# Performance work log

Hardware: AMD Instinct MI355X
Metric: run time of the kernel (lower is better)

Reference implementation:

```python
import jax, jax.numpy as jnp
import numpy as np
import math

N, V, NH = 4096, 256, 64  # samples, variables (channels), hidden units


def _permutation_skeleton(v):
    # perm[c] is a (V, V-1) selection matrix keeping all variables j != c,
    # columns ordered by j (faithful to CustomizedRelaModule.permutation_matrix
    # with skeleton = 1 - I, so max_dim = V - 1 and no zero-padding remains).
    perm = np.zeros((v, v, v - 1), dtype=np.float32)
    for c in range(v):
        idx = np.delete(np.arange(v), c)
        perm[c, idx, np.arange(v - 1)] = 1.0
    return jnp.asarray(perm)


def setup_inputs() -> dict:
    key = jax.random.key(0)
    k = jax.random.split(key, 7)
    data = jax.random.normal(k[0], (N, V), dtype=jnp.float32)
    adj = jax.random.normal(k[1], (V, V), dtype=jnp.float32)        # self.adj_matrix ~ N(0,1)
    neurons = jax.random.normal(k[2], (NH, V), dtype=jnp.float32)   # self.neurons ~ N(0,1)
    s1 = 1.0 / math.sqrt(V - 1)  # input_layer: uniform(-1/sqrt(in), 1/sqrt(in)), in = max_dim = V-1
    w_in = jax.random.uniform(k[3], (V, V - 1, NH), minval=-s1, maxval=s1, dtype=jnp.float32)
    b_in = jax.random.uniform(k[4], (V, NH), minval=-s1, maxval=s1, dtype=jnp.float32)
    s2 = 1.0 / math.sqrt(NH)
    w_out = jax.random.uniform(k[5], (V, NH, 1), minval=-s2, maxval=s2, dtype=jnp.float32)
    b_out = jax.random.uniform(k[6], (V, 1), minval=-s2, maxval=s2, dtype=jnp.float32)
    perm = _permutation_skeleton(V)
    return {"data": data, "adj": adj, "neurons": neurons,
            "w_in": w_in, "b_in": b_in, "w_out": w_out, "b_out": b_out,
            "perm": perm}


def reference(data, adj, neurons, w_in, b_in, w_out, b_out, perm):
    # categorical_matrix is identity, so the adjacency passed is adj itself.
    # Linear3D input layer with adj + permutation:
    #   masked[n, c, k] = sum_j data[n, j] * adj[j, c] * perm[c, j, k]
    # i.e. per channel c, gather adj-weighted inputs for all j != c.
    masked = jnp.einsum('nj,jc,cjk->nck', data, adj, perm)  # (N, V, V-1)
    # per-channel linear + tanh
    h = jnp.tanh(jnp.einsum('nck,ckh->nch', masked, w_in) + b_in[None])  # (N, V, NH)
    # output Linear3D with adj_matrix = neurons (NH, V): elementwise gate then per-channel linear
    gated = h * neurons.T[None]  # (N, V, NH)
    out = jnp.einsum('nch,cho->nco', gated, w_out) + b_out[None]  # (N, V, 1)
    return (adj, out[..., 0])
```

## Files before the change

kernel.cpp:

```cpp
#include <hip/hip_runtime.h>
#include <hip/hip_bf16.h>

#define NS   4096
#define NV   256
#define NHID 64
#define K2F  2.8853900817779268f

typedef short s8v __attribute__((ext_vector_type(8)));
typedef float f4v __attribute__((ext_vector_type(4)));

typedef __attribute__((address_space(1))) const unsigned int GU;
typedef __attribute__((address_space(3))) unsigned int LU;

__device__ __forceinline__ void gload16(const void* gp, void* lp) {
    __builtin_amdgcn_global_load_lds((GU*)gp, (LU*)lp, 16, 0, 0);
}

__device__ __forceinline__ unsigned short f2bf(float x) {
    __hip_bfloat16 h = __float2bfloat16(x);
    return *reinterpret_cast<unsigned short*>(&h);
}

__global__ __launch_bounds__(256) void k_prep_all(
        const float* __restrict__ adj, const float* __restrict__ w_in,
        unsigned short* __restrict__ W2t,
        const float* __restrict__ data, unsigned short* __restrict__ dataB,
        float* __restrict__ out0,
        const float* __restrict__ neurons, const float* __restrict__ w_out,
        const float* __restrict__ b_out, float* __restrict__ g2, float* __restrict__ BO,
        const float* __restrict__ b_in, float* __restrict__ bi2)
{
    __shared__ float t[64][65];
    const int blk = blockIdx.x, tid = threadIdx.x;
    if (blk < 1024) {
        int c  = blk >> 2;
        int k0 = (blk & 3) * 64;
#pragma unroll
        for (int i = 0; i < 16; ++i) {
            int lin = i * 256 + tid;
            int kr = lin >> 6, h = lin & 63;
            int k = k0 + kr;
            float v = 0.0f;
            if (k != c) {
                int m = k - (k > c ? 1 : 0);
                v = adj[k * NV + c] * w_in[((size_t)c * 255 + m) * 64 + h];
            }
            t[kr][h] = v;
        }
        __syncthreads();
#pragma unroll
        for (int i = 0; i < 16; ++i) {
            int lin = i * 256 + tid;
            int h = lin >> 6, kr = lin & 63;
            W2t[((size_t)(c * 64 + h)) * NV + k0 + kr] = f2bf(t[kr][h]);
        }
        return;
    }
    const int b = blk - 1024;
    if (b < 1024) {
        int i = b * 256 + tid;
        float4 v = reinterpret_cast<const float4*>(data)[i];
        ushort4 o = make_ushort4(f2bf(v.x), f2bf(v.y), f2bf(v.z), f2bf(v.w));
        reinterpret_cast<ushort4*>(dataB)[i] = o;
    } else if (b < 1088) {
        int i = (b - 1024) * 256 + tid;
        reinterpret_cast<float4*>(out0)[i] = reinterpret_cast<const float4*>(adj)[i];
    } else if (b < 1152) {
        int j = (b - 1088) * 256 + tid;
        int c = j >> 6, h = j & 63;
        float gv = neurons[h * NV + c] * w_out[j];
        g2[j] = 2.0f * gv;
        float s = gv;
        s += __shfl_xor(s, 1);  s += __shfl_xor(s, 2);  s += __shfl_xor(s, 4);
        s += __shfl_xor(s, 8);  s += __shfl_xor(s, 16); s += __shfl_xor(s, 32);
        if ((tid & 63) == 0) BO[c] = b_out[c] + s;
    } else {
        int i = (b - 1152) * 256 + tid;
        float4 v = reinterpret_cast<const float4*>(b_in)[i];
        v.x *= K2F; v.y *= K2F; v.z *= K2F; v.w *= K2F;
        reinterpret_cast<float4*>(bi2)[i] = v;
    }
}

__global__ __launch_bounds__(256, 3) void k_gemm_fused(
        const unsigned short* __restrict__ dataB,
        const unsigned short* __restrict__ W2t,
        const float* __restrict__ g2,
        const float* __restrict__ bi2,
        const float* __restrict__ BO,
        float* __restrict__ out1)
{
    __shared__ __align__(16) char lds[49152];
    const int tid  = threadIdx.x;
    const int w    = tid >> 6;
    const int lane = tid & 63;
    const int lq   = lane >> 4, lr = lane & 15;
    const int wr   = w >> 1, wc = w & 1;

    const int orig = (int)blockIdx.x;
    const int swz  = (orig & 7) * 512 + (orig >> 3);
    const int bm0  = (swz & 31) << 7;
    const int bn0  = (swz >> 5) << 7;

    f4v acc[4][4];
#pragma unroll
    for (int mi = 0; mi < 4; ++mi)
#pragma unroll
        for (int ni = 0; ni < 4; ++ni)
            acc[mi][ni] = (f4v){0.f, 0.f, 0.f, 0.f};

    const char* dA = (const char*)dataB;
    const char* dB = (const char*)W2t;
    const int rowt = tid >> 2;
    const int colb = (tid & 3) * 16;
    const char* srcA = dA + (size_t)(bm0 + rowt) * 512 + colb;
    const char* srcB = dB + (size_t)(bn0 + rowt) * 512 + colb;
    const unsigned ldst = (unsigned)(rowt * 64 + colb);

#define STAGE(KT, BUFO)                                                        \
    do {                                                                       \
        gload16(srcA + (KT) * 64,         lds + (BUFO) + ldst);                \
        gload16(srcA + 32768 + (KT) * 64, lds + (BUFO) + 4096 + ldst);         \
        gload16(srcB + (KT) * 64,         lds + (BUFO) + 8192 + ldst);         \
        gload16(srcB + 32768 + (KT) * 64, lds + (BUFO) + 12288 + ldst);        \
    } while (0)

    STAGE(0, 0);
    STAGE(1, 16384);

#pragma unroll
    for (int kt = 0; kt < 8; ++kt) {
        const int bufo = (kt % 3) * 16384;
        if (kt < 7) { asm volatile("s_waitcnt vmcnt(4)" ::: "memory"); }
        else        { asm volatile("s_waitcnt vmcnt(0)" ::: "memory"); }
        __builtin_amdgcn_sched_barrier(0);
        __builtin_amdgcn_s_barrier();
        __builtin_amdgcn_sched_barrier(0);
        if (kt < 6) STAGE(kt + 2, ((kt + 2) % 3) * 16384);

        s8v afr[4], bfr[4];
#pragma unroll
        for (int mi = 0; mi < 4; ++mi) {
            int ml = wr * 64 + mi * 16 + lr;
            afr[mi] = *reinterpret_cast<const s8v*>(lds + bufo + ml * 64 + lq * 16);
        }
#pragma unroll
        for (int ni = 0; ni < 4; ++ni) {
            int nl = wc * 64 + ni * 16 + lr;
            bfr[ni] = *reinterpret_cast<const s8v*>(lds + bufo + 8192 + nl * 64 + lq * 16);
        }
        __builtin_amdgcn_s_setprio(1);
#pragma unroll
        for (int mi = 0; mi < 4; ++mi)
#pragma unroll
            for (int ni = 0; ni < 4; ++ni)
                acc[mi][ni] = __builtin_amdgcn_mfma_f32_16x16x32_bf16(
                    bfr[ni], afr[mi], acc[mi][ni], 0, 0, 0);
        __builtin_amdgcn_s_setprio(0);
    }
#undef STAGE

    const int cidx = (bn0 >> 6) + wc;
    float4 g2v[4], bi2v[4];
#pragma unroll
    for (int ni = 0; ni < 4; ++ni) {
        int base = cidx * 64 + ni * 16 + lq * 4;
        g2v[ni]  = *(const float4*)&g2 [base];
        bi2v[ni] = *(const float4*)&bi2[base];
    }
    const float BOv = BO[cidx];

    float s0, s1, s2, s3;
#define EPI_TERM(T, GC, BC, RR)                                                \
    { float mm = __builtin_fmaf(acc[mi][ni][RR], K2F, (BC));                   \
      float e  = __builtin_amdgcn_exp2f(mm);                                   \
      (T) = __builtin_fmaf((GC), __builtin_amdgcn_rcpf(e + 1.0f), (T)); }
#define EPI_MI(T)                                                              \
    { float t = 0.f;                                                           \
      _Pragma("unroll")                                                        \
      for (int ni = 0; ni < 4; ++ni) {                                         \
          EPI_TERM(t, g2v[ni].x, bi2v[ni].x, 0);                               \
          EPI_TERM(t, g2v[ni].y, bi2v[ni].y, 1);                               \
          EPI_TERM(t, g2v[ni].z, bi2v[ni].z, 2);                               \
          EPI_TERM(t, g2v[ni].w, bi2v[ni].w, 3);                               \
      }                                                                        \
      t += __shfl_xor(t, 16);                                                  \
      t += __shfl_xor(t, 32);                                                  \
      (T) = t; }
    { const int mi = 0; EPI_MI(s0); }
    { const int mi = 1; EPI_MI(s1); }
    { const int mi = 2; EPI_MI(s2); }
    { const int mi = 3; EPI_MI(s3); }
#undef EPI_MI
#undef EPI_TERM
    float v = lane < 16 ? s0 : (lane < 32 ? s1 : (lane < 48 ? s2 : s3));
    out1[(unsigned)(bm0 + wr * 64 + lane) * NV + cidx] = BOv - v;
}

extern "C" void kernel_launch(void* const* d_in, const int* in_sizes, int n_in,
                              void* d_out, int out_size, void* d_ws, size_t ws_size,
                              hipStream_t stream) {
    const float* data    = (const float*)d_in[0];
    const float* adj     = (const float*)d_in[1];
    const float* neurons = (const float*)d_in[2];
    const float* w_in    = (const float*)d_in[3];
    const float* b_in    = (const float*)d_in[4];
    const float* w_out   = (const float*)d_in[5];
    const float* b_out   = (const float*)d_in[6];

    float* out0 = (float*)d_out;
    float* out1 = out0 + NV * NV;

    unsigned short* dataB = (unsigned short*)d_ws;
    unsigned short* W2t   = (unsigned short*)((char*)d_ws + 2097152);
    float*          g2    = (float*)((char*)d_ws + 10485760);
    float*          bi2   = (float*)((char*)d_ws + 10551296);
    float*          BO    = (float*)((char*)d_ws + 10616832);

    hipLaunchKernelGGL(k_prep_all, dim3(2192), dim3(256), 0, stream,
                       adj, w_in, W2t, data, dataB, out0,
                       neurons, w_out, b_out, g2, BO, b_in, bi2);
    hipLaunchKernelGGL(k_gemm_fused, dim3(4096), dim3(256), 0, stream,
                       dataB, W2t, g2, bi2, BO, out1);
}
```

Measured before the change: 60.02 us.

## Use 64-wide K tiles with XOR-swizzled LDS and double buffering

The GEMM main loop now stages 128-byte K slices (64 bf16) per tile instead of 64-byte slices, running 4 iterations instead of 8. It uses two 32 KB buffers instead of three 16 KB ones. The LDS rows are XOR-swizzled by row index to avoid bank conflicts on the 16-byte fragment reads. The change also adds a second barrier per iteration before refilling the just-consumed buffer, and raises LDS use to 64 KB per block, which may reduce occupancy below the launch-bounds target of 3 blocks.

```diff
diff --git a/kernel.cpp b/kernel.cpp
--- a/kernel.cpp
+++ b/kernel.cpp
@@ -90,7 +90,7 @@
         const float* __restrict__ BO,
         float* __restrict__ out1)
 {
-    __shared__ __align__(16) char lds[49152];
+    __shared__ __align__(16) char lds[65536];
     const int tid  = threadIdx.x;
     const int w    = tid >> 6;
     const int lane = tid & 63;
@@ -109,54 +109,71 @@
         for (int ni = 0; ni < 4; ++ni)
             acc[mi][ni] = (f4v){0.f, 0.f, 0.f, 0.f};
 
+    unsigned int offA[4], offB[4], ldso[4];
+#pragma unroll
+    for (int t = 0; t < 4; ++t) {
+        int o = w * 4096 + t * 1024 + lane * 16;
+        int row = o >> 7;
+        int inner = (o & 127) ^ ((row & 7) << 4);
+        ldso[t] = (unsigned)(w * 4096 + t * 1024);
+        offA[t] = (unsigned)(bm0 + row) * 512u + (unsigned)inner;
+        offB[t] = (unsigned)(bn0 + row) * 512u + (unsigned)inner;
+    }
+
     const char* dA = (const char*)dataB;
     const char* dB = (const char*)W2t;
-    const int rowt = tid >> 2;
-    const int colb = (tid & 3) * 16;
-    const char* srcA = dA + (size_t)(bm0 + rowt) * 512 + colb;
-    const char* srcB = dB + (size_t)(bn0 + rowt) * 512 + colb;
-    const unsigned ldst = (unsigned)(rowt * 64 + colb);
 
 #define STAGE(KT, BUFO)                                                        \
     do {                                                                       \
-        gload16(srcA + (KT) * 64,         lds + (BUFO) + ldst);                \
-        gload16(srcA + 32768 + (KT) * 64, lds + (BUFO) + 4096 + ldst);         \
-        gload16(srcB + (KT) * 64,         lds + (BUFO) + 8192 + ldst);         \
-        gload16(srcB + 32768 + (KT) * 64, lds + (BUFO) + 12288 + ldst);        \
+        _Pragma("unroll")                                                      \
+        for (int t = 0; t < 4; ++t)                                            \
+            gload16(dA + (size_t)offA[t] + (KT) * 128, lds + (BUFO) + ldso[t]); \
+        _Pragma("unroll")                                                      \
+        for (int t = 0; t < 4; ++t)                                            \
+            gload16(dB + (size_t)offB[t] + (KT) * 128, lds + (BUFO) + 16384 + ldso[t]); \
     } while (0)
 
     STAGE(0, 0);
-    STAGE(1, 16384);
-
-#pragma unroll
-    for (int kt = 0; kt < 8; ++kt) {
-        const int bufo = (kt % 3) * 16384;
-        if (kt < 7) { asm volatile("s_waitcnt vmcnt(4)" ::: "memory"); }
+    STAGE(1, 32768);
+
+#pragma unroll
+    for (int kt = 0; kt < 4; ++kt) {
+        const int bufo = (kt & 1) << 15;
+        if (kt < 3) { asm volatile("s_waitcnt vmcnt(8)" ::: "memory"); }
         else        { asm volatile("s_waitcnt vmcnt(0)" ::: "memory"); }
         __builtin_amdgcn_sched_barrier(0);
         __builtin_amdgcn_s_barrier();
         __builtin_amdgcn_sched_barrier(0);
-        if (kt < 6) STAGE(kt + 2, ((kt + 2) % 3) * 16384);
-
-        s8v afr[4], bfr[4];
-#pragma unroll
-        for (int mi = 0; mi < 4; ++mi) {
-            int ml = wr * 64 + mi * 16 + lr;
-            afr[mi] = *reinterpret_cast<const s8v*>(lds + bufo + ml * 64 + lq * 16);
+
+#pragma unroll
+        for (int kk = 0; kk < 2; ++kk) {
+            s8v afr[4], bfr[4];
+#pragma unroll
+            for (int mi = 0; mi < 4; ++mi) {
+                int ml = wr * 64 + mi * 16 + lr;
+                int inner = (kk * 64 + (lq << 4)) ^ ((ml & 7) << 4);
+                afr[mi] = *reinterpret_cast<const s8v*>(lds + bufo + ml * 128 + inner);
+            }
+#pragma unroll
+            for (int ni = 0; ni < 4; ++ni) {
+                int nl = wc * 64 + ni * 16 + lr;
+                int inner = (kk * 64 + (lq << 4)) ^ ((nl & 7) << 4);
+                bfr[ni] = *reinterpret_cast<const s8v*>(lds + bufo + 16384 + nl * 128 + inner);
+            }
+            __builtin_amdgcn_s_setprio(1);
+#pragma unroll
+            for (int mi = 0; mi < 4; ++mi)
+#pragma unroll
+                for (int ni = 0; ni < 4; ++ni)
+                    acc[mi][ni] = __builtin_amdgcn_mfma_f32_16x16x32_bf16(
+                        bfr[ni], afr[mi], acc[mi][ni], 0, 0, 0);
+            __builtin_amdgcn_s_setprio(0);
         }
-#pragma unroll
-        for (int ni = 0; ni < 4; ++ni) {
-            int nl = wc * 64 + ni * 16 + lr;
-            bfr[ni] = *reinterpret_cast<const s8v*>(lds + bufo + 8192 + nl * 64 + lq * 16);
-        }
-        __builtin_amdgcn_s_setprio(1);
-#pragma unroll
-        for (int mi = 0; mi < 4; ++mi)
-#pragma unroll
-            for (int ni = 0; ni < 4; ++ni)
-                acc[mi][ni] = __builtin_amdgcn_mfma_f32_16x16x32_bf16(
-                    bfr[ni], afr[mi], acc[mi][ni], 0, 0, 0);
-        __builtin_amdgcn_s_setprio(0);
+
+        __builtin_amdgcn_sched_barrier(0);
+        __builtin_amdgcn_s_barrier();
+        __builtin_amdgcn_sched_barrier(0);
+        if (kt < 2) STAGE(kt + 2, bufo);
     }
 #undef STAGE
 
```

New measurement: 62.78 us. 4.6% more time.
